# Kernel tuning notes

Measured on AMD Instinct MI355X. Metric: run time of the kernel, lower is better.

The kernel has to match this reference:

```python
import jax, jax.numpy as jnp
import numpy as np

B = 512
N = 8732  # SSD300 default box count, hard-coded in the original asserts


def point_form(boxes):
    # (cx, cy, w, h) -> (xmin, ymin, xmax, ymax), as in the original repo
    return jnp.concatenate([boxes[..., :2] - boxes[..., 2:] / 2,
                            boxes[..., :2] + boxes[..., 2:] / 2], axis=-1)


def setup_inputs() -> dict:
    key = jax.random.key(0)
    k1, k2, k3, k4, k5 = jax.random.split(key, 5)
    ploc = jax.random.normal(k1, (B, 4, N), jnp.float32)
    pconf = jax.random.normal(k2, (B, 2, N), jnp.float32)
    # ground-truth boxes: keep w/h strictly positive for the log in _to_offsets
    gloc = jax.random.uniform(k3, (B, N, 4), jnp.float32, minval=0.05, maxval=1.0)
    glabel = (jax.random.uniform(k4, (B, N)) < 0.02).astype(jnp.int32)
    # default boxes in cxcywh; keep away from 0 so point_form xmax/ymax > 0
    dboxes = jax.random.uniform(k5, (N, 4), jnp.float32, minval=0.2, maxval=0.8)
    return {"ploc": ploc, "pconf": pconf, "gloc": gloc, "glabel": glabel, "dboxes": dboxes}


def reference(ploc, pconf, gloc, glabel, dboxes):
    db = point_form(dboxes)                      # [N,4]
    dxy, dwh = db[:, :2], db[:, 2:]              # faithful to original indexing
    # offset encode ground truth
    gxy = (gloc[..., :2] - dxy) / dwh            # [B,N,2]
    gwh = jnp.log(gloc[..., 2:] / dwh)           # [B,N,2]
    goff = jnp.concatenate([gxy, gwh], axis=-1)  # [B,N,4]

    pl = jnp.swapaxes(ploc, 1, 2)                # [B,N,4]
    diff = pl - goff
    ad = jnp.abs(diff)
    sl1 = jnp.where(ad < 1.0, 0.5 * diff * diff, ad - 0.5).sum(-1)  # [B,N]

    mask = glabel > 0                            # [B,N]
    pos = mask.sum(axis=1)                       # [B]
    loc_loss = jnp.where(mask, sl1, 0.0).sum(axis=1)

    # per-anchor cross entropy over the class dim
    logp = jax.nn.log_softmax(pconf, axis=1)     # [B,2,N]
    closs = -jnp.take_along_axis(logp, glabel[:, None, :], axis=1)[:, 0, :]  # [B,N]

    # hard negative mining: rank negatives by loss via double argsort
    con_neg = jnp.where(mask, 0.0, closs)
    con_idx = jnp.argsort(-con_neg, axis=1)
    con_rank = jnp.argsort(con_idx, axis=1)
    neg_num = jnp.minimum(3 * pos, N)[:, None]
    neg_mask = con_rank < neg_num
    w = mask.astype(closs.dtype) + neg_mask.astype(closs.dtype)
    con_loss = (closs * w).sum(axis=1)

    total = loc_loss + con_loss
    num_mask = (pos > 0).astype(total.dtype)
    posf = jnp.maximum(pos.astype(total.dtype), 1e-6)
    return (total * num_mask / posf).mean()
```

## Files before the change

### kernel.cpp

```cpp
#include <hip/hip_runtime.h>
#include <cstdint>

#define BLOCK 512
#define NWAVES 8
#define B_SZ 512
#define N_SZ 8732
#define NG (N_SZ/4)

__device__ __forceinline__ float f4c(const float4& v, int j) {
  return j==0 ? v.x : (j==1 ? v.y : (j==2 ? v.z : v.w));
}
__device__ __forceinline__ int i4c(const int4& v, int j) {
  return j==0 ? v.x : (j==1 ? v.y : (j==2 ? v.z : v.w));
}
__device__ __forceinline__ float smoothl1(float d) {
  float ad = fabsf(d);
  return ad < 1.0f ? 0.5f*d*d : ad - 0.5f;
}

__global__ __launch_bounds__(BLOCK, 4)
void mbl_row_kernel(const float* __restrict__ ploc,
                    const float* __restrict__ pconf,
                    const float* __restrict__ gloc,
                    const int*   __restrict__ glabel,
                    const float* __restrict__ dboxes,
                    float* __restrict__ rowout)
{
  __shared__ __align__(16) uint32_t con[N_SZ];
  __shared__ uint32_t hist[NWAVES*256];
  __shared__ uint32_t scan[256];
  __shared__ float redf[NWAVES], redf2[NWAVES];
  __shared__ int   redi[NWAVES];
  __shared__ int sh_pos, sh_rem;
  __shared__ uint32_t sh_prefix;
  __shared__ float sh_loc, sh_pcl;

  const int b   = blockIdx.x;
  const int tid = threadIdx.x;
  const int wid = tid >> 6;
  const int lane = tid & 63;

  const float* pl  = ploc  + (size_t)b * (4*N_SZ);
  const float* pc  = pconf + (size_t)b * (2*N_SZ);
  const float4* gl4  = (const float4*)(gloc   + (size_t)b * (N_SZ*4));
  const int4*   lab4 = (const int4*)  (glabel + (size_t)b * N_SZ);
  const float4* db4  = (const float4*)dboxes;

  float loc_acc = 0.f, pcl_acc = 0.f;
  int pos_acc = 0;

  for (int g = tid; g < NG; g += BLOCK) {
    const int n = g*4;
    float4 pl0 = *(const float4*)(pl + n);
    float4 pl1 = *(const float4*)(pl + N_SZ   + n);
    float4 pl2 = *(const float4*)(pl + 2*N_SZ + n);
    float4 pl3 = *(const float4*)(pl + 3*N_SZ + n);
    float4 pc0 = *(const float4*)(pc + n);
    float4 pc1 = *(const float4*)(pc + N_SZ + n);
    int4 lb = lab4[g];
    uint32_t cw[4];
    #pragma unroll
    for (int j = 0; j < 4; ++j) {
      float4 g4 = gl4[n + j];
      float4 d4 = db4[n + j];
      float dxy0 = d4.x - 0.5f*d4.z;
      float dxy1 = d4.y - 0.5f*d4.w;
      float dwh0 = d4.x + 0.5f*d4.z;
      float dwh1 = d4.y + 0.5f*d4.w;
      float go0 = (g4.x - dxy0) / dwh0;
      float go1 = (g4.y - dxy1) / dwh1;
      float go2 = logf(g4.z / dwh0);
      float go3 = logf(g4.w / dwh1);
      float s = smoothl1(f4c(pl0,j) - go0)
              + smoothl1(f4c(pl1,j) - go1)
              + smoothl1(f4c(pl2,j) - go2)
              + smoothl1(f4c(pl3,j) - go3);
      float x0 = f4c(pc0,j), x1 = f4c(pc1,j);
      float mx  = fmaxf(x0, x1);
      float lse = mx + logf(expf(x0-mx) + expf(x1-mx));
      int L = i4c(lb, j);
      float closs = lse - (L ? x1 : x0);
      if (L > 0) {
        pos_acc += 1;
        loc_acc += s;
        pcl_acc += closs;
        cw[j] = 0u;
      } else {
        cw[j] = __float_as_uint(closs);
      }
    }
    ((uint4*)con)[g] = make_uint4(cw[0], cw[1], cw[2], cw[3]);
  }

  #pragma unroll
  for (int off = 32; off; off >>= 1) {
    loc_acc += __shfl_down(loc_acc, off);
    pcl_acc += __shfl_down(pcl_acc, off);
    pos_acc += __shfl_down(pos_acc, off);
  }
  if (lane == 0) { redf[wid] = loc_acc; redf2[wid] = pcl_acc; redi[wid] = pos_acc; }
  __syncthreads();
  if (tid == 0) {
    float lsum = 0.f, psum = 0.f; int ps = 0;
    for (int w = 0; w < NWAVES; ++w) { lsum += redf[w]; psum += redf2[w]; ps += redi[w]; }
    sh_loc = lsum; sh_pcl = psum; sh_pos = ps;
    sh_prefix = 0u;
    int K = 3*ps; if (K > N_SZ) K = N_SZ;
    sh_rem = K;
  }
  __syncthreads();

  const int pos = sh_pos;
  if (pos > 0) {
    for (int shift = 24; shift >= 0; shift -= 8) {
      for (int i = tid; i < NWAVES*256; i += BLOCK) hist[i] = 0u;
      __syncthreads();
      const uint32_t pref  = sh_prefix;
      const uint32_t pmask = (shift == 24) ? 0u : (0xFFFFFFFFu << (shift+8));
      const int rem = sh_rem;
      uint32_t* h = hist + wid*256;
      for (int n = tid; n < N_SZ; n += BLOCK) {
        uint32_t bits = con[n];
        if ((bits & pmask) == pref)
          atomicAdd(&h[(bits >> shift) & 255u], 1u);
      }
      __syncthreads();
      if (tid < 256) {
        uint32_t s = 0;
        #pragma unroll
        for (int w = 0; w < NWAVES; ++w) s += hist[w*256 + tid];
        scan[tid] = s;
      }
      __syncthreads();
      for (int d = 1; d < 256; d <<= 1) {
        uint32_t v = 0;
        if (tid < 256 && tid + d < 256) v = scan[tid + d];
        __syncthreads();
        if (tid < 256) scan[tid] += v;
        __syncthreads();
      }
      if (tid < 256) {
        int sj = (int)scan[tid];
        int sn = (tid < 255) ? (int)scan[tid+1] : 0;
        if (sj >= rem && sn < rem) {
          sh_prefix = pref | ((uint32_t)tid << shift);
          sh_rem = rem - sn;
        }
      }
      __syncthreads();
    }

    const uint32_t tbits = sh_prefix;
    const int ties = sh_rem;
    float sg = 0.f;
    for (int n = tid; n < N_SZ; n += BLOCK) {
      uint32_t bits = con[n];
      if (bits > tbits) sg += __uint_as_float(bits);
    }
    #pragma unroll
    for (int off = 32; off; off >>= 1) sg += __shfl_down(sg, off);
    if (lane == 0) redf[wid] = sg;
    __syncthreads();
    if (tid == 0) {
      float sum_gt = 0.f;
      for (int w = 0; w < NWAVES; ++w) sum_gt += redf[w];
      float con_loss = sh_pcl + sum_gt + (float)ties * __uint_as_float(tbits);
      float total = sh_loc + con_loss;
      rowout[b] = total / (float)pos;
    }
  } else {
    if (tid == 0) rowout[b] = 0.f;
  }
}

__global__ void mbl_reduce(const float* __restrict__ rowv, float* __restrict__ out) {
  __shared__ float red[NWAVES];
  const int tid = threadIdx.x;
  float v = (tid < B_SZ) ? rowv[tid] : 0.f;
  #pragma unroll
  for (int off = 32; off; off >>= 1) v += __shfl_down(v, off);
  if ((tid & 63) == 0) red[tid >> 6] = v;
  __syncthreads();
  if (tid == 0) {
    float s = 0.f;
    for (int w = 0; w < NWAVES; ++w) s += red[w];
    out[0] = s / (float)B_SZ;
  }
}

extern "C" void kernel_launch(void* const* d_in, const int* in_sizes, int n_in,
                              void* d_out, int out_size, void* d_ws, size_t ws_size,
                              hipStream_t stream) {
  const float* ploc   = (const float*)d_in[0];
  const float* pconf  = (const float*)d_in[1];
  const float* gloc   = (const float*)d_in[2];
  const int*   glabel = (const int*)  d_in[3];
  const float* dboxes = (const float*)d_in[4];
  float* rowv = (float*)d_ws;

  hipLaunchKernelGGL(mbl_row_kernel, dim3(B_SZ), dim3(BLOCK), 0, stream,
                     ploc, pconf, gloc, glabel, dboxes, rowv);
  hipLaunchKernelGGL(mbl_reduce, dim3(1), dim3(BLOCK), 0, stream,
                     rowv, (float*)d_out);
}
```

Before: 208.1 us.

## Fuse first radix histogram into loss pass, use fast math and wave-level scan

Builds the top-byte histogram for the radix select during the main loss loop, so one full pass over shared memory is skipped. The 256-bin block scan with many barriers becomes a single-wave shuffle suffix scan. Block size doubles to 1024 threads while histogram copies stay at 8. Division, log and exp use fast intrinsics and softmax CE is rewritten as softplus, trading a little accuracy for fewer instructions.

```diff
diff --git a/kernel.cpp b/kernel.cpp
--- a/kernel.cpp
+++ b/kernel.cpp
@@ -1,8 +1,9 @@
 #include <hip/hip_runtime.h>
 #include <cstdint>
 
-#define BLOCK 512
-#define NWAVES 8
+#define BLOCK 1024
+#define NWAVES (BLOCK/64)
+#define NHIST 8
 #define B_SZ 512
 #define N_SZ 8732
 #define NG (N_SZ/4)
@@ -18,7 +19,7 @@
   return ad < 1.0f ? 0.5f*d*d : ad - 0.5f;
 }
 
-__global__ __launch_bounds__(BLOCK, 4)
+__global__ __launch_bounds__(BLOCK, 8)
 void mbl_row_kernel(const float* __restrict__ ploc,
                     const float* __restrict__ pconf,
                     const float* __restrict__ gloc,
@@ -27,17 +28,16 @@
                     float* __restrict__ rowout)
 {
   __shared__ __align__(16) uint32_t con[N_SZ];
-  __shared__ uint32_t hist[NWAVES*256];
-  __shared__ uint32_t scan[256];
+  __shared__ uint32_t hist[NHIST*256];
   __shared__ float redf[NWAVES], redf2[NWAVES];
   __shared__ int   redi[NWAVES];
   __shared__ int sh_pos, sh_rem;
   __shared__ uint32_t sh_prefix;
   __shared__ float sh_loc, sh_pcl;
 
-  const int b   = blockIdx.x;
-  const int tid = threadIdx.x;
-  const int wid = tid >> 6;
+  const int b    = blockIdx.x;
+  const int tid  = threadIdx.x;
+  const int wid  = tid >> 6;
   const int lane = tid & 63;
 
   const float* pl  = ploc  + (size_t)b * (4*N_SZ);
@@ -46,8 +46,12 @@
   const int4*   lab4 = (const int4*)  (glabel + (size_t)b * N_SZ);
   const float4* db4  = (const float4*)dboxes;
 
+  for (int i = tid; i < NHIST*256; i += BLOCK) hist[i] = 0u;
+  __syncthreads();
+
   float loc_acc = 0.f, pcl_acc = 0.f;
   int pos_acc = 0;
+  uint32_t* hmy = hist + (wid & (NHIST-1))*256;
 
   for (int g = tid; g < NG; g += BLOCK) {
     const int n = g*4;
@@ -67,19 +71,19 @@
       float dxy1 = d4.y - 0.5f*d4.w;
       float dwh0 = d4.x + 0.5f*d4.z;
       float dwh1 = d4.y + 0.5f*d4.w;
-      float go0 = (g4.x - dxy0) / dwh0;
-      float go1 = (g4.y - dxy1) / dwh1;
-      float go2 = logf(g4.z / dwh0);
-      float go3 = logf(g4.w / dwh1);
+      float go0 = __fdividef(g4.x - dxy0, dwh0);
+      float go1 = __fdividef(g4.y - dxy1, dwh1);
+      float go2 = __logf(__fdividef(g4.z, dwh0));
+      float go3 = __logf(__fdividef(g4.w, dwh1));
       float s = smoothl1(f4c(pl0,j) - go0)
               + smoothl1(f4c(pl1,j) - go1)
               + smoothl1(f4c(pl2,j) - go2)
               + smoothl1(f4c(pl3,j) - go3);
       float x0 = f4c(pc0,j), x1 = f4c(pc1,j);
-      float mx  = fmaxf(x0, x1);
-      float lse = mx + logf(expf(x0-mx) + expf(x1-mx));
+      float d  = x1 - x0;
+      float sp = __logf(1.0f + __expf(-fabsf(d)));
       int L = i4c(lb, j);
-      float closs = lse - (L ? x1 : x0);
+      float closs = sp + (L ? fmaxf(-d, 0.f) : fmaxf(d, 0.f));
       if (L > 0) {
         pos_acc += 1;
         loc_acc += s;
@@ -90,6 +94,10 @@
       }
     }
     ((uint4*)con)[g] = make_uint4(cw[0], cw[1], cw[2], cw[3]);
+    atomicAdd(&hmy[cw[0] >> 24], 1u);
+    atomicAdd(&hmy[cw[1] >> 24], 1u);
+    atomicAdd(&hmy[cw[2] >> 24], 1u);
+    atomicAdd(&hmy[cw[3] >> 24], 1u);
   }
 
   #pragma unroll
@@ -113,39 +121,43 @@
   const int pos = sh_pos;
   if (pos > 0) {
     for (int shift = 24; shift >= 0; shift -= 8) {
-      for (int i = tid; i < NWAVES*256; i += BLOCK) hist[i] = 0u;
-      __syncthreads();
-      const uint32_t pref  = sh_prefix;
-      const uint32_t pmask = (shift == 24) ? 0u : (0xFFFFFFFFu << (shift+8));
-      const int rem = sh_rem;
-      uint32_t* h = hist + wid*256;
-      for (int n = tid; n < N_SZ; n += BLOCK) {
-        uint32_t bits = con[n];
-        if ((bits & pmask) == pref)
-          atomicAdd(&h[(bits >> shift) & 255u], 1u);
-      }
-      __syncthreads();
-      if (tid < 256) {
-        uint32_t s = 0;
-        #pragma unroll
-        for (int w = 0; w < NWAVES; ++w) s += hist[w*256 + tid];
-        scan[tid] = s;
-      }
-      __syncthreads();
-      for (int d = 1; d < 256; d <<= 1) {
-        uint32_t v = 0;
-        if (tid < 256 && tid + d < 256) v = scan[tid + d];
+      if (shift != 24) {
+        for (int i = tid; i < NHIST*256; i += BLOCK) hist[i] = 0u;
         __syncthreads();
-        if (tid < 256) scan[tid] += v;
+        const uint32_t pref  = sh_prefix;
+        const uint32_t pmask = 0xFFFFFFFFu << (shift+8);
+        for (int n = tid; n < N_SZ; n += BLOCK) {
+          uint32_t bits = con[n];
+          if ((bits & pmask) == pref)
+            atomicAdd(&hmy[(bits >> shift) & 255u], 1u);
+        }
         __syncthreads();
       }
-      if (tid < 256) {
-        int sj = (int)scan[tid];
-        int sn = (tid < 255) ? (int)scan[tid+1] : 0;
-        if (sj >= rem && sn < rem) {
-          sh_prefix = pref | ((uint32_t)tid << shift);
-          sh_rem = rem - sn;
+      if (wid == 0) {
+        uint32_t c0 = 0, c1 = 0, c2 = 0, c3 = 0;
+        #pragma unroll
+        for (int w = 0; w < NHIST; ++w) {
+          const uint32_t* h = hist + w*256 + 4*lane;
+          c0 += h[0]; c1 += h[1]; c2 += h[2]; c3 += h[3];
         }
+        uint32_t sl = c0 + c1 + c2 + c3;
+        uint32_t suf = sl;
+        #pragma unroll
+        for (int off = 1; off < 64; off <<= 1) {
+          uint32_t v = __shfl_down(suf, off);
+          if (lane + off < 64) suf += v;
+        }
+        uint32_t ex = suf - sl;
+        uint32_t s3 = ex + c3;
+        uint32_t s2 = s3 + c2;
+        uint32_t s1 = s2 + c1;
+        uint32_t s0 = s1 + c0;
+        const uint32_t rem  = (uint32_t)sh_rem;
+        const uint32_t pref = sh_prefix;
+        if (s0 >= rem && s1 < rem) { sh_prefix = pref | ((uint32_t)(4*lane  ) << shift); sh_rem = (int)(rem - s1); }
+        if (s1 >= rem && s2 < rem) { sh_prefix = pref | ((uint32_t)(4*lane+1) << shift); sh_rem = (int)(rem - s2); }
+        if (s2 >= rem && s3 < rem) { sh_prefix = pref | ((uint32_t)(4*lane+2) << shift); sh_rem = (int)(rem - s3); }
+        if (s3 >= rem && ex < rem) { sh_prefix = pref | ((uint32_t)(4*lane+3) << shift); sh_rem = (int)(rem - ex); }
       }
       __syncthreads();
     }
@@ -174,7 +186,7 @@
 }
 
 __global__ void mbl_reduce(const float* __restrict__ rowv, float* __restrict__ out) {
-  __shared__ float red[NWAVES];
+  __shared__ float red[8];
   const int tid = threadIdx.x;
   float v = (tid < B_SZ) ? rowv[tid] : 0.f;
   #pragma unroll
@@ -183,7 +195,7 @@
   __syncthreads();
   if (tid == 0) {
     float s = 0.f;
-    for (int w = 0; w < NWAVES; ++w) s += red[w];
+    for (int w = 0; w < 8; ++w) s += red[w];
     out[0] = s / (float)B_SZ;
   }
 }
@@ -200,6 +212,6 @@
 
   hipLaunchKernelGGL(mbl_row_kernel, dim3(B_SZ), dim3(BLOCK), 0, stream,
                      ploc, pconf, gloc, glabel, dboxes, rowv);
-  hipLaunchKernelGGL(mbl_reduce, dim3(1), dim3(BLOCK), 0, stream,
+  hipLaunchKernelGGL(mbl_reduce, dim3(1), dim3(512), 0, stream,
                      rowv, (float*)d_out);
 }
```

New measurement: 197.5 us. -5.1%, faster.
